# Performance work log

Hardware: AMD Instinct MI355X
Metric: run time of the kernel (lower is better)

Reference implementation:

```python
import jax, jax.numpy as jnp
import numpy as np
from jax import lax

C = 192; H = W = T = 32; WS = 4; SS = 2; NH = 6; HD = C // NH
N = WS ** 3; NB = 4; HIDDEN = 4 * C; OUT = 192


def _rel_index():
    c = np.stack(np.meshgrid(np.arange(WS), np.arange(WS), np.arange(WS), indexing='ij')).reshape(3, -1)
    r = (c[:, :, None] - c[:, None, :]).transpose(1, 2, 0) + (WS - 1)
    return (r[..., 0] * (2 * WS - 1) ** 2 + r[..., 1] * (2 * WS - 1) + r[..., 2]).astype(np.int32)  # (N,N)


def _attn_mask():
    m = np.zeros((H, W, T), np.float32)
    sl = [slice(0, -WS), slice(-WS, -SS), slice(-SS, None)]
    cnt = 0
    for hs in sl:
        for ws_ in sl:
            for ts in sl:
                m[hs, ws_, ts] = cnt
                cnt += 1
    mw = m.reshape(H // WS, WS, W // WS, WS, T // WS, WS).transpose(0, 2, 4, 1, 3, 5).reshape(-1, N)
    am = mw[:, None, :] - mw[:, :, None]  # (nW,N,N)
    return np.where(am != 0, -100.0, 0.0).astype(np.float32)

_RPI = _rel_index()
_MASK = _attn_mask()


def _ln(x, g, b):
    mu = x.mean(-1, keepdims=True)
    v = ((x - mu) ** 2).mean(-1, keepdims=True)
    return (x - mu) / jnp.sqrt(v + 1e-5) * g + b


def _partition(x):  # (B,H,W,T,C) -> (B*nW,N,C)
    b = x.shape[0]
    x = x.reshape(b, H // WS, WS, W // WS, WS, T // WS, WS, C)
    return x.transpose(0, 1, 3, 5, 2, 4, 6, 7).reshape(-1, N, C)


def _reverse(w, b):  # (B*nW,N,C) -> (B,H,W,T,C)
    x = w.reshape(b, H // WS, W // WS, T // WS, WS, WS, WS, C)
    return x.transpose(0, 1, 4, 2, 5, 3, 6, 7).reshape(b, H, W, T, C)


def _swin_block(xf, shifted, p, mask):
    (n1g, n1b, qw, qb, rp, pw, pb, n2g, n2b, f1w, f1b, f2w, f2b) = p
    b = xf.shape[0]
    shortcut = xf
    h = _ln(xf, n1g, n1b).reshape(b, H, W, T, C)
    if shifted:
        h = jnp.roll(h, (-SS, -SS, -SS), (1, 2, 3))
    wins = _partition(h)  # (b*nW,N,C)
    qkv = (wins @ qw + qb).reshape(-1, N, 3, NH, HD).transpose(2, 0, 3, 1, 4)
    q, k, v = qkv[0], qkv[1], qkv[2]  # (b*nW,NH,N,HD)
    attn = jnp.einsum('bhnd,bhmd->bhnm', q * (HD ** -0.5), k)
    attn = attn + rp[_RPI].transpose(2, 0, 1)[None]  # + rel-pos bias (NH,N,N)
    if shifted:
        nW = mask.shape[0]
        attn = (attn.reshape(b, nW, NH, N, N) + mask[None, :, None]).reshape(-1, NH, N, N)
    attn = jax.nn.softmax(attn, -1)
    o = jnp.einsum('bhnm,bhmd->bhnd', attn, v).transpose(0, 2, 1, 3).reshape(-1, N, C)
    o = o @ pw + pb
    h = _reverse(o, b)
    if shifted:
        h = jnp.roll(h, (SS, SS, SS), (1, 2, 3))
    xf = shortcut + h.reshape(b, -1, C)
    z = _ln(xf, n2g, n2b)
    z = jax.nn.gelu(z @ f1w + f1b, approximate=False) @ f2w + f2b
    return xf + z


def _forward(x, norm1_g, norm1_b, qkv_w, qkv_b, rpb, proj_w, proj_b,
             norm2_g, norm2_b, fc1_w, fc1_b, fc2_w, fc2_b,
             dw_w, dw_b, pw_w, pw_b, bn_g, bn_b):
    b = x.shape[0]
    xf = x.reshape(b, C, -1).transpose(0, 2, 1)  # b (h w t) c
    mask = jnp.asarray(_MASK)
    for i in range(NB):
        p = (norm1_g[i], norm1_b[i], qkv_w[i], qkv_b[i], rpb[i], proj_w[i], proj_b[i],
             norm2_g[i], norm2_b[i], fc1_w[i], fc1_b[i], fc2_w[i], fc2_b[i])
        xf = _swin_block(xf, i % 2 == 1, p, mask)
    y = xf.transpose(0, 2, 1).reshape(b, C, H, W, T)
    # refine: depthwise 3x3x3 + pointwise 1x1x1 conv, eval-mode BN (mean 0, var 1), ReLU
    dn = ('NCDHW', 'OIDHW', 'NCDHW')
    y = lax.conv_general_dilated(y, dw_w, (1, 1, 1), [(1, 1)] * 3,
                                 dimension_numbers=dn, feature_group_count=C) + dw_b.reshape(1, -1, 1, 1, 1)
    y = lax.conv_general_dilated(y, pw_w, (1, 1, 1), [(0, 0)] * 3,
                                 dimension_numbers=dn) + pw_b.reshape(1, -1, 1, 1, 1)
    y = y / jnp.sqrt(1.0 + 1e-5) * bn_g.reshape(1, -1, 1, 1, 1) + bn_b.reshape(1, -1, 1, 1, 1)
    return jax.nn.relu(y)


def setup_inputs() -> dict:
    ks = jax.random.split(jax.random.key(0), 12)
    s = 0.02
    return {
        'x': jax.random.normal(ks[0], (2, C, H, W, T), jnp.float32),
        'norm1_g': jnp.ones((NB, C)), 'norm1_b': jnp.zeros((NB, C)),
        'qkv_w': jax.random.normal(ks[1], (NB, C, 3 * C)) * s, 'qkv_b': jnp.zeros((NB, 3 * C)),
        'rpb': jax.random.normal(ks[2], (NB, (2 * WS - 1) ** 3, NH)) * s,
        'proj_w': jax.random.normal(ks[3], (NB, C, C)) * s, 'proj_b': jnp.zeros((NB, C)),
        'norm2_g': jnp.ones((NB, C)), 'norm2_b': jnp.zeros((NB, C)),
        'fc1_w': jax.random.normal(ks[4], (NB, C, HIDDEN)) * s, 'fc1_b': jnp.zeros((NB, HIDDEN)),
        'fc2_w': jax.random.normal(ks[5], (NB, HIDDEN, C)) * s, 'fc2_b': jnp.zeros((NB, C)),
        'dw_w': jax.random.normal(ks[6], (C, 1, 3, 3, 3)) * 0.1, 'dw_b': jnp.zeros((C,)),
        'pw_w': jax.random.normal(ks[7], (OUT, C, 1, 1, 1)) * 0.05, 'pw_b': jnp.zeros((OUT,)),
        'bn_g': jnp.ones((OUT,)), 'bn_b': jnp.zeros((OUT,)),
    }


def reference(x, norm1_g, norm1_b, qkv_w, qkv_b, rpb, proj_w, proj_b,
              norm2_g, norm2_b, fc1_w, fc1_b, fc2_w, fc2_b,
              dw_w, dw_b, pw_w, pw_b, bn_g, bn_b):
    return _forward(x, norm1_g, norm1_b, qkv_w, qkv_b, rpb, proj_w, proj_b,
                    norm2_g, norm2_b, fc1_w, fc1_b, fc2_w, fc2_b,
                    dw_w, dw_b, pw_w, pw_b, bn_g, bn_b)
```

## Files before the change

kernel.cpp:

```cpp
#include <hip/hip_runtime.h>
#include <hip/hip_bf16.h>

#define DI __device__ __forceinline__

typedef short bf16x8 __attribute__((ext_vector_type(8)));
typedef float f32x4 __attribute__((ext_vector_type(4)));
typedef short s16x4 __attribute__((ext_vector_type(4)));

DI short f2bf(float f) {
    __hip_bfloat16 h = __float2bfloat16(f);
    return *reinterpret_cast<short*>(&h);
}

DI void gload_lds16(const short* gsrc, short* ldst) {
    __builtin_amdgcn_global_load_lds(
        (const __attribute__((address_space(1))) void*)gsrc,
        (__attribute__((address_space(3))) void*)ldst, 16, 0, 0);
}

DI int reg3(int p) { return p < 28 ? 0 : (p < 30 ? 1 : 2); }

__global__ __launch_bounds__(256) void transpose_in(const float* __restrict__ x,
                                                    float* __restrict__ xf) {
    __shared__ float tile[32][33];
    int b = blockIdx.z;
    int c0 = blockIdx.y * 32;
    int l0 = blockIdx.x * 32;
    int tx = threadIdx.x, ty = threadIdx.y;
#pragma unroll
    for (int i = 0; i < 32; i += 8)
        tile[ty + i][tx] = x[(long)(b * 192 + c0 + ty + i) * 32768 + l0 + tx];
    __syncthreads();
#pragma unroll
    for (int i = 0; i < 32; i += 8)
        xf[(long)(b * 32768 + l0 + ty + i) * 192 + c0 + tx] = tile[tx][ty + i];
}

__global__ __launch_bounds__(256) void prep_w(const float* __restrict__ qkv_w,
                                              const float* __restrict__ proj_w,
                                              const float* __restrict__ fc1_w,
                                              const float* __restrict__ fc2_w,
                                              const float* __restrict__ pw_w,
                                              short* __restrict__ wt) {
    int i = blockIdx.x * 256 + threadIdx.x;
    float v;
    if (i < 1769472) {
        int b4 = i / 442368, r = i - b4 * 442368;
        if (r < 110592) { int n = r / 192, k = r - n * 192; v = qkv_w[b4 * 110592 + k * 576 + n]; }
        else if (r < 147456) { int r2 = r - 110592; int n = r2 / 192, k = r2 - n * 192; v = proj_w[b4 * 36864 + k * 192 + n]; }
        else if (r < 294912) { int r2 = r - 147456; int n = r2 / 192, k = r2 - n * 192; v = fc1_w[b4 * 147456 + k * 768 + n]; }
        else { int r2 = r - 294912; int n = r2 / 768, k = r2 - n * 768; v = fc2_w[b4 * 147456 + k * 192 + n]; }
        wt[i] = f2bf(v);
    } else {
        int r = i - 1769472;
        wt[i] = f2bf(pw_w[r]);
    }
}

template <bool PART>
__global__ __launch_bounds__(256) void ln_k(const float* __restrict__ xf,
                                            const float* __restrict__ g,
                                            const float* __restrict__ bta,
                                            short* __restrict__ out, int shift) {
    int wv = threadIdx.x >> 6, lane = threadIdx.x & 63;
    int row = blockIdx.x * 4 + wv;
    long src;
    if (PART) {
        int b = row >> 15, r = row & 32767, widx = r >> 6, n = r & 63;
        int wh = widx >> 6, ww = (widx >> 3) & 7, wt = widx & 7;
        int ih = n >> 4, iw = (n >> 2) & 3, it = n & 3;
        int h = ((wh << 2) + ih + shift) & 31;
        int w = ((ww << 2) + iw + shift) & 31;
        int t = ((wt << 2) + it + shift) & 31;
        src = ((long)(b << 15) + (h << 10) + (w << 5) + t) * 192;
    } else {
        src = (long)row * 192;
    }
    float v[3], s = 0.f, sq = 0.f;
#pragma unroll
    for (int j = 0; j < 3; j++) {
        v[j] = xf[src + lane + 64 * j];
        s += v[j];
        sq += v[j] * v[j];
    }
#pragma unroll
    for (int o = 1; o < 64; o <<= 1) {
        s += __shfl_xor(s, o, 64);
        sq += __shfl_xor(sq, o, 64);
    }
    float mu = s * (1.f / 192.f);
    float var = sq * (1.f / 192.f) - mu * mu;
    float rstd = rsqrtf(var + 1e-5f);
    long dst = (long)row * 192;
#pragma unroll
    for (int j = 0; j < 3; j++) {
        int c = lane + 64 * j;
        out[dst + c] = f2bf((v[j] - mu) * rstd * g[c] + bta[c]);
    }
}

template <int MODE>
__global__ __launch_bounds__(256) void gemm_k(
    const short* __restrict__ A, const short* __restrict__ Bt,
    const float* __restrict__ bias,
    short* __restrict__ outB, float* __restrict__ resid, float* __restrict__ outF,
    const float* __restrict__ bng, const float* __restrict__ bnb,
    int M, int N, int K, int shift) {
    __shared__ short As[128 * 64];
    __shared__ short Bs[64 * 64];
    const int tid = threadIdx.x;
    const int nwg = gridDim.x;
    const int wg = ((blockIdx.x & 7) * (nwg >> 3)) + (blockIdx.x >> 3);
    const int tiles_n = N >> 6;
    const int m0 = (wg / tiles_n) << 7;
    const int n0 = (wg % tiles_n) << 6;
    const int wv = tid >> 6, lane = tid & 63;
    const int lr = lane & 15, lg = lane >> 4;
    const int srow = lane >> 3;
    const int scb = ((lane & 7) ^ (lane >> 3)) << 3;

    f32x4 acc[2][4] = {};
    for (int kt = 0; kt < K; kt += 64) {
        __syncthreads();
#pragma unroll
        for (int i = 0; i < 4; i++) {
            int rbase = i * 32 + wv * 8;
            gload_lds16(A + (long)(m0 + rbase + srow) * K + kt + scb, As + rbase * 64);
        }
#pragma unroll
        for (int i = 0; i < 2; i++) {
            int rbase = i * 32 + wv * 8;
            gload_lds16(Bt + (long)(n0 + rbase + srow) * K + kt + scb, Bs + rbase * 64);
        }
        __syncthreads();
#pragma unroll
        for (int ks = 0; ks < 2; ks++) {
            bf16x8 af[2], bfv[4];
            int kb = (ks << 2) + lg;
#pragma unroll
            for (int mi = 0; mi < 2; mi++) {
                int r = (wv << 5) + (mi << 4) + lr;
                af[mi] = *(const bf16x8*)(As + r * 64 + ((kb ^ (r & 7)) << 3));
            }
#pragma unroll
            for (int ni = 0; ni < 4; ni++) {
                int r = (ni << 4) + lr;
                bfv[ni] = *(const bf16x8*)(Bs + r * 64 + ((kb ^ (r & 7)) << 3));
            }
#pragma unroll
            for (int mi = 0; mi < 2; mi++)
#pragma unroll
                for (int ni = 0; ni < 4; ni++)
                    acc[mi][ni] = __builtin_amdgcn_mfma_f32_16x16x32_bf16(
                        af[mi], bfv[ni], acc[mi][ni], 0, 0, 0);
        }
    }

#pragma unroll
    for (int mi = 0; mi < 2; mi++) {
        int rbase = m0 + (wv << 5) + (mi << 4) + (lg << 2);
#pragma unroll
        for (int ni = 0; ni < 4; ni++) {
            int col = n0 + (ni << 4) + lr;
            float bv = bias[col];
            if (MODE == 4) {
                float sc = 0.9999950000374997f * bng[col];
                float bb = bnb[col];
                f32x4 o;
#pragma unroll
                for (int e = 0; e < 4; e++) {
                    float v = (acc[mi][ni][e] + bv) * sc + bb;
                    o[e] = v > 0.f ? v : 0.f;
                }
                int b = rbase >> 15, l = rbase & 32767;
                *(f32x4*)(outF + ((long)(b * 192 + col) << 15) + l) = o;
            } else {
#pragma unroll
                for (int e = 0; e < 4; e++) {
                    int r = rbase + e;
                    float v = acc[mi][ni][e] + bv;
                    if (MODE == 0) {
                        outB[(long)r * N + col] = f2bf(v);
                    } else {
                        int b = r >> 15, rr = r & 32767, widx = rr >> 6, n = rr & 63;
                        int wh = widx >> 6, ww = (widx >> 3) & 7, wt = widx & 7;
                        int ih = n >> 4, iw = (n >> 2) & 3, it = n & 3;
                        int h = ((wh << 2) + ih + shift) & 31;
                        int w = ((ww << 2) + iw + shift) & 31;
                        int t = ((wt << 2) + it + shift) & 31;
                        long tok = (long)(b << 15) + (h << 10) + (w << 5) + t;
                        resid[tok * 192 + col] += v;
                    }
                }
            }
        }
    }
}

__global__ __launch_bounds__(512, 2) void mlp_k(const float* __restrict__ XF,
                                                const short* __restrict__ W1g,
                                                const short* __restrict__ W2g,
                                                const float* __restrict__ b1,
                                                const float* __restrict__ b2,
                                                const float* __restrict__ n2g,
                                                const float* __restrict__ n2b,
                                                float* __restrict__ resid) {
    __shared__ short Wbuf[2][24576];
    __shared__ short Hs[16384];
    const int tid = threadIdx.x;
    const int wv = tid >> 6, lane = tid & 63;
    const int lr = lane & 15, lg = lane >> 4;
    const int mt = ((blockIdx.x & 7) << 5) + (blockIdx.x >> 3);
    const int m0 = mt << 8;
    short* hw = Hs + (wv << 11);

    bf16x8 areg[2][6];
#pragma unroll
    for (int mf = 0; mf < 2; mf++) {
        const float* rp = XF + (long)(m0 + (wv << 5) + (mf << 4) + lr) * 192;
        f32x4 xv[6][2];
        float s = 0.f, sq = 0.f;
#pragma unroll
        for (int kk = 0; kk < 6; kk++)
#pragma unroll
            for (int q = 0; q < 2; q++) {
                xv[kk][q] = *(const f32x4*)(rp + kk * 32 + (lg << 3) + q * 4);
#pragma unroll
                for (int e = 0; e < 4; e++) {
                    s += xv[kk][q][e];
                    sq += xv[kk][q][e] * xv[kk][q][e];
                }
            }
        s += __shfl_xor(s, 16, 64); s += __shfl_xor(s, 32, 64);
        sq += __shfl_xor(sq, 16, 64); sq += __shfl_xor(sq, 32, 64);
        float mu = s * (1.f / 192.f);
        float var = sq * (1.f / 192.f) - mu * mu;
        float rstd = rsqrtf(var + 1e-5f);
#pragma unroll
        for (int kk = 0; kk < 6; kk++) {
            int cb = kk * 32 + (lg << 3);
            f32x4 g0 = *(const f32x4*)(n2g + cb), g1 = *(const f32x4*)(n2g + cb + 4);
            f32x4 b0 = *(const f32x4*)(n2b + cb), b1v = *(const f32x4*)(n2b + cb + 4);
            bf16x8 t;
#pragma unroll
            for (int e = 0; e < 4; e++) {
                t[e] = f2bf((xv[kk][0][e] - mu) * rstd * g0[e] + b0[e]);
                t[e + 4] = f2bf((xv[kk][1][e] - mu) * rstd * g1[e] + b1v[e]);
            }
            areg[mf][kk] = t;
        }
    }

    auto stage = [&](int jc, int buf) {
#pragma unroll
        for (int q = 0; q < 3; q++) {
            int base = (wv * 3 + q) * 512;
            int E = base + lane * 8;
            int row = E / 192;
            int cb = (E - row * 192) >> 3;
            gload_lds16(W1g + (long)(jc * 64 + row) * 192 + ((cb ^ (row & 7)) << 3),
                        &Wbuf[buf][base]);
        }
#pragma unroll
        for (int q = 0; q < 3; q++) {
            int base = (wv * 3 + q) * 512;
            int E = base + lane * 8;
            int row = E >> 6;
            int cb = (E & 63) >> 3;
            gload_lds16(W2g + (long)row * 768 + jc * 64 + ((cb ^ (row & 7)) << 3),
                        &Wbuf[buf][12288 + base]);
        }
    };

    stage(0, 0);
    __syncthreads();

    f32x4 acc[2][12] = {};

    for (int j = 0; j < 12; j++) {
        if (j < 11) stage(j + 1, (j + 1) & 1);
        const short* W1s = Wbuf[j & 1];
        const short* W2s = Wbuf[j & 1] + 12288;

        f32x4 hacc[4][2] = {};
#pragma unroll
        for (int kk = 0; kk < 6; kk++) {
            int cb = (kk << 2) + lg;
            bf16x8 wf[4];
#pragma unroll
            for (int hf = 0; hf < 4; hf++) {
                int r = (hf << 4) + lr;
                wf[hf] = *(const bf16x8*)(W1s + r * 192 + ((cb ^ (r & 7)) << 3));
            }
#pragma unroll
            for (int hf = 0; hf < 4; hf++)
#pragma unroll
                for (int mf = 0; mf < 2; mf++)
                    hacc[hf][mf] = __builtin_amdgcn_mfma_f32_16x16x32_bf16(
                        wf[hf], areg[mf][kk], hacc[hf][mf], 0, 0, 0);
        }

#pragma unroll
        for (int hf = 0; hf < 4; hf++) {
            f32x4 bv = *(const f32x4*)(b1 + j * 64 + (hf << 4) + (lg << 2));
#pragma unroll
            for (int mf = 0; mf < 2; mf++) {
                s16x4 hv;
#pragma unroll
                for (int e = 0; e < 4; e++) {
                    float v = hacc[hf][mf][e] + bv[e];
                    float inner = fmaf(-0.07135481627f, v * v, -1.595769122f);
                    float eterm = __expf(v * inner);
                    float gl = v * __builtin_amdgcn_rcpf(1.f + eterm);
                    hv[e] = f2bf(gl);
                }
                int Mrow = (mf << 4) + lr;
                int blk = (hf << 1) | (lg >> 1);
                *(s16x4*)(hw + Mrow * 64 + ((blk ^ (Mrow & 7)) << 3) + ((lg & 1) << 2)) = hv;
            }
        }
        asm volatile("s_waitcnt lgkmcnt(0)" ::: "memory");

#pragma unroll
        for (int kk = 0; kk < 2; kk++) {
            int cb = (kk << 2) + lg;
            bf16x8 ah[2], bw[12];
#pragma unroll
            for (int mf = 0; mf < 2; mf++) {
                int r = (mf << 4) + lr;
                ah[mf] = *(const bf16x8*)(hw + r * 64 + ((cb ^ (r & 7)) << 3));
            }
#pragma unroll
            for (int nj = 0; nj < 12; nj++) {
                int r = (nj << 4) + lr;
                bw[nj] = *(const bf16x8*)(W2s + r * 64 + ((cb ^ (r & 7)) << 3));
            }
#pragma unroll
            for (int mf = 0; mf < 2; mf++)
#pragma unroll
                for (int nj = 0; nj < 12; nj++)
                    acc[mf][nj] = __builtin_amdgcn_mfma_f32_16x16x32_bf16(
                        ah[mf], bw[nj], acc[mf][nj], 0, 0, 0);
        }
        __syncthreads();
    }

#pragma unroll
    for (int mf = 0; mf < 2; mf++) {
        int rbase = m0 + (wv << 5) + (mf << 4) + (lg << 2);
#pragma unroll
        for (int nj = 0; nj < 12; nj++) {
            int col = (nj << 4) + lr;
            float bv = b2[col];
#pragma unroll
            for (int e = 0; e < 4; e++) {
                long r = rbase + e;
                resid[r * 192 + col] += acc[mf][nj][e] + bv;
            }
        }
    }
}

__global__ __launch_bounds__(256) void attn_k(const short* __restrict__ qkv,
                                              const float* __restrict__ rpb,
                                              short* __restrict__ o, int shifted) {
    __shared__ short lds[4 * 6144];
    const int wv = threadIdx.x >> 6, lane = threadIdx.x & 63;
    short* vT = lds + wv * 6144;
    short* P = lds + wv * 6144 + 2048;
    const int task = blockIdx.x * 4 + wv;
    const int win = task / 6, head = task - win * 6;
    const int lr = lane & 15, lg = lane >> 4;
    const long qbase = (long)win * 64 * 576 + head * 32;

    bf16x8 aq[4], bk[4];
#pragma unroll
    for (int bi = 0; bi < 4; bi++)
        aq[bi] = *(const bf16x8*)(qkv + qbase + (long)((bi << 4) + lr) * 576 + (lg << 3));
#pragma unroll
    for (int bj = 0; bj < 4; bj++)
        bk[bj] = *(const bf16x8*)(qkv + qbase + 192 + (long)((bj << 4) + lr) * 576 + (lg << 3));
    f32x4 s[4][4] = {};
#pragma unroll
    for (int bi = 0; bi < 4; bi++)
#pragma unroll
        for (int bj = 0; bj < 4; bj++)
            s[bi][bj] = __builtin_amdgcn_mfma_f32_16x16x32_bf16(aq[bi], bk[bj], s[bi][bj], 0, 0, 0);

#pragma unroll
    for (int j = 0; j < 4; j++) {
        bf16x8 vv = *(const bf16x8*)(qkv + qbase + 384 + (long)lane * 576 + (j << 3));
#pragma unroll
        for (int e = 0; e < 8; e++) {
            int d = (j << 3) + e;
            vT[d * 64 + (((lane >> 3) ^ (d & 7)) << 3) + (lane & 7)] = vv[e];
        }
    }

    const float SCALE = 0.17677669529663687f;
    int widx = win & 511;
    int wh = widx >> 6, ww = (widx >> 3) & 7, wt = widx & 7;
    int ihm[4], iwm[4], itm[4], lblm[4];
#pragma unroll
    for (int bj = 0; bj < 4; bj++) {
        int m = (bj << 4) + lr;
        ihm[bj] = m >> 4; iwm[bj] = (m >> 2) & 3; itm[bj] = m & 3;
        lblm[bj] = reg3((wh << 2) + ihm[bj]) * 9 + reg3((ww << 2) + iwm[bj]) * 3 + reg3((wt << 2) + itm[bj]);
    }
#pragma unroll
    for (int bi = 0; bi < 4; bi++) {
#pragma unroll
        for (int e = 0; e < 4; e++) {
            int n = (bi << 4) + (lg << 2) + e;
            int ihn = n >> 4, iwn = (n >> 2) & 3, itn = n & 3;
            int lbln = reg3((wh << 2) + ihn) * 9 + reg3((ww << 2) + iwn) * 3 + reg3((wt << 2) + itn);
#pragma unroll
            for (int bj = 0; bj < 4; bj++) {
                int idx = (ihn - ihm[bj] + 3) * 49 + (iwn - iwm[bj] + 3) * 7 + (itn - itm[bj] + 3);
                float bias = rpb[idx * 6 + head];
                float val = s[bi][bj][e] * SCALE + bias;
                if (shifted && lbln != lblm[bj]) val -= 100.f;
                s[bi][bj][e] = val;
            }
        }
    }

#pragma unroll
    for (int bi = 0; bi < 4; bi++) {
#pragma unroll
        for (int e = 0; e < 4; e++) {
            float mx = s[bi][0][e];
#pragma unroll
            for (int bj = 1; bj < 4; bj++) mx = fmaxf(mx, s[bi][bj][e]);
#pragma unroll
            for (int off = 1; off < 16; off <<= 1) mx = fmaxf(mx, __shfl_xor(mx, off, 64));
            float sm = 0.f;
#pragma unroll
            for (int bj = 0; bj < 4; bj++) {
                float p = __expf(s[bi][bj][e] - mx);
                s[bi][bj][e] = p;
                sm += p;
            }
#pragma unroll
            for (int off = 1; off < 16; off <<= 1) sm += __shfl_xor(sm, off, 64);
            float rinv = 1.f / sm;
            int n = (bi << 4) + (lg << 2) + e;
#pragma unroll
            for (int bj = 0; bj < 4; bj++) {
                int m = (bj << 4) + lr;
                P[n * 64 + (((m >> 3) ^ (n & 7)) << 3) + (m & 7)] = f2bf(s[bi][bj][e] * rinv);
            }
        }
    }

    f32x4 oacc[4][2] = {};
#pragma unroll
    for (int ks = 0; ks < 2; ks++) {
        bf16x8 ap[4], bv2[2];
        int kb = (ks << 2) + lg;
#pragma unroll
        for (int bi = 0; bi < 4; bi++) {
            int r = (bi << 4) + lr;
            ap[bi] = *(const bf16x8*)(P + r * 64 + ((kb ^ (r & 7)) << 3));
        }
#pragma unroll
        for (int nf = 0; nf < 2; nf++) {
            int d = (nf << 4) + lr;
            bv2[nf] = *(const bf16x8*)(vT + d * 64 + ((kb ^ (d & 7)) << 3));
        }
#pragma unroll
        for (int bi = 0; bi < 4; bi++)
#pragma unroll
            for (int nf = 0; nf < 2; nf++)
                oacc[bi][nf] = __builtin_amdgcn_mfma_f32_16x16x32_bf16(ap[bi], bv2[nf], oacc[bi][nf], 0, 0, 0);
    }
#pragma unroll
    for (int bi = 0; bi < 4; bi++)
#pragma unroll
        for (int nf = 0; nf < 2; nf++)
#pragma unroll
            for (int e = 0; e < 4; e++) {
                int n = (bi << 4) + (lg << 2) + e;
                int d = (nf << 4) + lr;
                o[((long)win * 64 + n) * 192 + head * 32 + d] = f2bf(oacc[bi][nf][e]);
            }
}

__global__ __launch_bounds__(192) void dw_k(const float* __restrict__ xf,
                                            const float* __restrict__ w,
                                            const float* __restrict__ db,
                                            short* __restrict__ out) {
    int c = threadIdx.x;
    int blk = blockIdx.x;
    int t0 = (blk & 3) << 3;
    int bhw = blk >> 2;
    int b = bhw >> 10, h = (bhw >> 5) & 31, wq = bhw & 31;

    float wr[27];
#pragma unroll
    for (int k = 0; k < 27; k++) wr[k] = w[c * 27 + k];
    float bias = db[c];
    float acc[8];
#pragma unroll
    for (int j = 0; j < 8; j++) acc[j] = bias;

#pragma unroll
    for (int a = 0; a < 3; a++) {
        int hh = h + a - 1;
        if (hh < 0 || hh > 31) continue;
#pragma unroll
        for (int bb = 0; bb < 3; bb++) {
            int ww = wq + bb - 1;
            if (ww < 0 || ww > 31) continue;
            const float* base = xf + ((long)(b << 15) + (hh << 10) + (ww << 5)) * 192 + c;
            float val[10];
#pragma unroll
            for (int tt = 0; tt < 10; tt++) {
                int t = t0 + tt - 1;
                val[tt] = (t >= 0 && t < 32) ? base[t * 192] : 0.f;
            }
#pragma unroll
            for (int d = 0; d < 3; d++) {
                float wv = wr[a * 9 + bb * 3 + d];
#pragma unroll
                for (int j = 0; j < 8; j++)
                    acc[j] = fmaf(val[j + d], wv, acc[j]);
            }
        }
    }
    long obase = ((long)(b << 15) + (h << 10) + (wq << 5) + t0) * 192 + c;
#pragma unroll
    for (int j = 0; j < 8; j++) out[obase + j * 192] = f2bf(acc[j]);
}

extern "C" void kernel_launch(void* const* d_in, const int* in_sizes, int n_in,
                              void* d_out, int out_size, void* d_ws, size_t ws_size,
                              hipStream_t stream) {
    const float* x      = (const float*)d_in[0];
    const float* n1g    = (const float*)d_in[1];
    const float* n1b    = (const float*)d_in[2];
    const float* qkv_w  = (const float*)d_in[3];
    const float* qkv_b  = (const float*)d_in[4];
    const float* rpb    = (const float*)d_in[5];
    const float* proj_w = (const float*)d_in[6];
    const float* proj_b = (const float*)d_in[7];
    const float* n2g    = (const float*)d_in[8];
    const float* n2b    = (const float*)d_in[9];
    const float* fc1_w  = (const float*)d_in[10];
    const float* fc1_b  = (const float*)d_in[11];
    const float* fc2_w  = (const float*)d_in[12];
    const float* fc2_b  = (const float*)d_in[13];
    const float* dw_w   = (const float*)d_in[14];
    const float* dw_b   = (const float*)d_in[15];
    const float* pw_w   = (const float*)d_in[16];
    const float* pw_b   = (const float*)d_in[17];
    const float* bn_g   = (const float*)d_in[18];
    const float* bn_b   = (const float*)d_in[19];
    float* outF = (float*)d_out;

    char* ws = (char*)d_ws;
    float* XF = (float*)ws;
    short* Abuf = (short*)(ws + 50331648);
    short* Bbuf = (short*)(ws + 150994944);
    short* WT = (short*)(ws + 226492416);

    transpose_in<<<dim3(1024, 6, 2), dim3(32, 8), 0, stream>>>(x, XF);
    prep_w<<<7056, 256, 0, stream>>>(qkv_w, proj_w, fc1_w, fc2_w, pw_w, WT);

    for (int i = 0; i < 4; i++) {
        int shifted = i & 1;
        int shift = shifted ? 2 : 0;
        ln_k<true><<<16384, 256, 0, stream>>>(XF, n1g + i * 192, n1b + i * 192, Abuf, shift);
        gemm_k<0><<<4608, 256, 0, stream>>>(Abuf, WT + (long)i * 442368, qkv_b + i * 576,
                                            Bbuf, nullptr, nullptr, nullptr, nullptr,
                                            65536, 576, 192, 0);
        attn_k<<<1536, 256, 0, stream>>>(Bbuf, rpb + i * 2058, Abuf, shifted);
        gemm_k<3><<<1536, 256, 0, stream>>>(Abuf, WT + (long)i * 442368 + 110592, proj_b + i * 192,
                                            nullptr, XF, nullptr, nullptr, nullptr,
                                            65536, 192, 192, shift);
        mlp_k<<<256, 512, 0, stream>>>(XF, WT + (long)i * 442368 + 147456,
                                       WT + (long)i * 442368 + 294912,
                                       fc1_b + i * 768, fc2_b + i * 192,
                                       n2g + i * 192, n2b + i * 192, XF);
    }

    dw_k<<<8192, 192, 0, stream>>>(XF, dw_w, dw_b, Abuf);
    gemm_k<4><<<1536, 256, 0, stream>>>(Abuf, WT + 1769472, pw_b,
                                        nullptr, nullptr, outF, bn_g, bn_b,
                                        65536, 192, 192, 0);
}
```

Measured before the change: 766.5 us.

## Fuse LayerNorm into QKV GEMM and use full-weight-resident GEMMs for K=192

Replaces the separate LayerNorm kernel plus generic QKV GEMM with one kernel that loads window-partitioned rows, normalizes them in registers, keeps the A tile in registers and streams 64-column weight chunks through double-buffered LDS. The proj and final pointwise GEMMs become a kernel that holds the entire 192x192 weight in LDS and computes all 192 output columns per 128-row tile, so A is read once. This removes the LN round trip through global memory, one launch per block, and repeated A reloads across N tiles, at the cost of fewer, larger workgroups (512) with more registers and LDS per block.

```diff
diff --git a/kernel.cpp b/kernel.cpp
--- a/kernel.cpp
+++ b/kernel.cpp
@@ -57,111 +57,173 @@
     }
 }
 
-template <bool PART>
-__global__ __launch_bounds__(256) void ln_k(const float* __restrict__ xf,
-                                            const float* __restrict__ g,
-                                            const float* __restrict__ bta,
-                                            short* __restrict__ out, int shift) {
-    int wv = threadIdx.x >> 6, lane = threadIdx.x & 63;
-    int row = blockIdx.x * 4 + wv;
-    long src;
-    if (PART) {
+__global__ __launch_bounds__(256) void qkv_k(const float* __restrict__ XF,
+                                             const short* __restrict__ Wg,
+                                             const float* __restrict__ bias,
+                                             const float* __restrict__ n1g,
+                                             const float* __restrict__ n1b,
+                                             short* __restrict__ out, int shift) {
+    __shared__ short Ws[2][12288];
+    const int tid = threadIdx.x;
+    const int wv = tid >> 6, lane = tid & 63;
+    const int lr = lane & 15, lg = lane >> 4;
+    const int mt = ((blockIdx.x & 7) << 6) + (blockIdx.x >> 3);
+    const int m0 = mt << 7;
+
+    bf16x8 areg[2][6];
+#pragma unroll
+    for (int mf = 0; mf < 2; mf++) {
+        int row = m0 + (wv << 5) + (mf << 4) + lr;
         int b = row >> 15, r = row & 32767, widx = r >> 6, n = r & 63;
         int wh = widx >> 6, ww = (widx >> 3) & 7, wt = widx & 7;
         int ih = n >> 4, iw = (n >> 2) & 3, it = n & 3;
         int h = ((wh << 2) + ih + shift) & 31;
         int w = ((ww << 2) + iw + shift) & 31;
         int t = ((wt << 2) + it + shift) & 31;
-        src = ((long)(b << 15) + (h << 10) + (w << 5) + t) * 192;
-    } else {
-        src = (long)row * 192;
-    }
-    float v[3], s = 0.f, sq = 0.f;
-#pragma unroll
-    for (int j = 0; j < 3; j++) {
-        v[j] = xf[src + lane + 64 * j];
-        s += v[j];
-        sq += v[j] * v[j];
-    }
-#pragma unroll
-    for (int o = 1; o < 64; o <<= 1) {
-        s += __shfl_xor(s, o, 64);
-        sq += __shfl_xor(sq, o, 64);
-    }
-    float mu = s * (1.f / 192.f);
-    float var = sq * (1.f / 192.f) - mu * mu;
-    float rstd = rsqrtf(var + 1e-5f);
-    long dst = (long)row * 192;
-#pragma unroll
-    for (int j = 0; j < 3; j++) {
-        int c = lane + 64 * j;
-        out[dst + c] = f2bf((v[j] - mu) * rstd * g[c] + bta[c]);
+        const float* rp = XF + ((long)(b << 15) + (h << 10) + (w << 5) + t) * 192;
+        f32x4 xv[6][2];
+        float s = 0.f, sq = 0.f;
+#pragma unroll
+        for (int kk = 0; kk < 6; kk++)
+#pragma unroll
+            for (int q = 0; q < 2; q++) {
+                xv[kk][q] = *(const f32x4*)(rp + kk * 32 + (lg << 3) + q * 4);
+#pragma unroll
+                for (int e = 0; e < 4; e++) {
+                    s += xv[kk][q][e];
+                    sq += xv[kk][q][e] * xv[kk][q][e];
+                }
+            }
+        s += __shfl_xor(s, 16, 64); s += __shfl_xor(s, 32, 64);
+        sq += __shfl_xor(sq, 16, 64); sq += __shfl_xor(sq, 32, 64);
+        float mu = s * (1.f / 192.f);
+        float var = sq * (1.f / 192.f) - mu * mu;
+        float rstd = rsqrtf(var + 1e-5f);
+#pragma unroll
+        for (int kk = 0; kk < 6; kk++) {
+            int cb = kk * 32 + (lg << 3);
+            f32x4 g0 = *(const f32x4*)(n1g + cb), g1 = *(const f32x4*)(n1g + cb + 4);
+            f32x4 b0 = *(const f32x4*)(n1b + cb), b1v = *(const f32x4*)(n1b + cb + 4);
+            bf16x8 tt;
+#pragma unroll
+            for (int e = 0; e < 4; e++) {
+                tt[e] = f2bf((xv[kk][0][e] - mu) * rstd * g0[e] + b0[e]);
+                tt[e + 4] = f2bf((xv[kk][1][e] - mu) * rstd * g1[e] + b1v[e]);
+            }
+            areg[mf][kk] = tt;
+        }
+    }
+
+    auto stage = [&](int jc, int buf) {
+#pragma unroll
+        for (int q = 0; q < 6; q++) {
+            int base = (wv * 6 + q) * 512;
+            int E = base + lane * 8;
+            int row = E / 192;
+            int cb = (E - row * 192) >> 3;
+            gload_lds16(Wg + (long)(jc * 64 + row) * 192 + ((cb ^ (row & 7)) << 3),
+                        &Ws[buf][base]);
+        }
+    };
+
+    stage(0, 0);
+    __syncthreads();
+
+    for (int j = 0; j < 9; j++) {
+        if (j < 8) stage(j + 1, (j + 1) & 1);
+        const short* W = Ws[j & 1];
+        f32x4 acc[2][4] = {};
+#pragma unroll
+        for (int kk = 0; kk < 6; kk++) {
+            int cb = (kk << 2) + lg;
+            bf16x8 wf[4];
+#pragma unroll
+            for (int nf = 0; nf < 4; nf++) {
+                int r = (nf << 4) + lr;
+                wf[nf] = *(const bf16x8*)(W + r * 192 + ((cb ^ (r & 7)) << 3));
+            }
+#pragma unroll
+            for (int mf = 0; mf < 2; mf++)
+#pragma unroll
+                for (int nf = 0; nf < 4; nf++)
+                    acc[mf][nf] = __builtin_amdgcn_mfma_f32_16x16x32_bf16(
+                        areg[mf][kk], wf[nf], acc[mf][nf], 0, 0, 0);
+        }
+#pragma unroll
+        for (int mf = 0; mf < 2; mf++) {
+#pragma unroll
+            for (int nf = 0; nf < 4; nf++) {
+                int col = j * 64 + (nf << 4) + lr;
+                float bv = bias[col];
+#pragma unroll
+                for (int e = 0; e < 4; e++) {
+                    int row = m0 + (wv << 5) + (mf << 4) + (lg << 2) + e;
+                    out[(long)row * 576 + col] = f2bf(acc[mf][nf][e] + bv);
+                }
+            }
+        }
+        __syncthreads();
     }
 }
 
 template <int MODE>
-__global__ __launch_bounds__(256) void gemm_k(
-    const short* __restrict__ A, const short* __restrict__ Bt,
-    const float* __restrict__ bias,
-    short* __restrict__ outB, float* __restrict__ resid, float* __restrict__ outF,
-    const float* __restrict__ bng, const float* __restrict__ bnb,
-    int M, int N, int K, int shift) {
-    __shared__ short As[128 * 64];
-    __shared__ short Bs[64 * 64];
+__global__ __launch_bounds__(256) void wk_k(const short* __restrict__ A,
+                                            const short* __restrict__ Wg,
+                                            const float* __restrict__ bias,
+                                            float* __restrict__ resid, float* __restrict__ outF,
+                                            const float* __restrict__ bng,
+                                            const float* __restrict__ bnb, int shift) {
+    __shared__ short Ws[36864];
     const int tid = threadIdx.x;
-    const int nwg = gridDim.x;
-    const int wg = ((blockIdx.x & 7) * (nwg >> 3)) + (blockIdx.x >> 3);
-    const int tiles_n = N >> 6;
-    const int m0 = (wg / tiles_n) << 7;
-    const int n0 = (wg % tiles_n) << 6;
     const int wv = tid >> 6, lane = tid & 63;
     const int lr = lane & 15, lg = lane >> 4;
-    const int srow = lane >> 3;
-    const int scb = ((lane & 7) ^ (lane >> 3)) << 3;
-
-    f32x4 acc[2][4] = {};
-    for (int kt = 0; kt < K; kt += 64) {
-        __syncthreads();
-#pragma unroll
-        for (int i = 0; i < 4; i++) {
-            int rbase = i * 32 + wv * 8;
-            gload_lds16(A + (long)(m0 + rbase + srow) * K + kt + scb, As + rbase * 64);
-        }
-#pragma unroll
-        for (int i = 0; i < 2; i++) {
-            int rbase = i * 32 + wv * 8;
-            gload_lds16(Bt + (long)(n0 + rbase + srow) * K + kt + scb, Bs + rbase * 64);
-        }
-        __syncthreads();
-#pragma unroll
-        for (int ks = 0; ks < 2; ks++) {
-            bf16x8 af[2], bfv[4];
-            int kb = (ks << 2) + lg;
-#pragma unroll
-            for (int mi = 0; mi < 2; mi++) {
-                int r = (wv << 5) + (mi << 4) + lr;
-                af[mi] = *(const bf16x8*)(As + r * 64 + ((kb ^ (r & 7)) << 3));
-            }
-#pragma unroll
-            for (int ni = 0; ni < 4; ni++) {
-                int r = (ni << 4) + lr;
-                bfv[ni] = *(const bf16x8*)(Bs + r * 64 + ((kb ^ (r & 7)) << 3));
-            }
-#pragma unroll
-            for (int mi = 0; mi < 2; mi++)
-#pragma unroll
-                for (int ni = 0; ni < 4; ni++)
-                    acc[mi][ni] = __builtin_amdgcn_mfma_f32_16x16x32_bf16(
-                        af[mi], bfv[ni], acc[mi][ni], 0, 0, 0);
-        }
-    }
-
-#pragma unroll
-    for (int mi = 0; mi < 2; mi++) {
-        int rbase = m0 + (wv << 5) + (mi << 4) + (lg << 2);
-#pragma unroll
-        for (int ni = 0; ni < 4; ni++) {
-            int col = n0 + (ni << 4) + lr;
+    const int mt = ((blockIdx.x & 7) << 6) + (blockIdx.x >> 3);
+    const int m0 = mt << 7;
+
+    bf16x8 areg[2][6];
+#pragma unroll
+    for (int mf = 0; mf < 2; mf++)
+#pragma unroll
+        for (int kk = 0; kk < 6; kk++)
+            areg[mf][kk] = *(const bf16x8*)(A + (long)(m0 + (wv << 5) + (mf << 4) + lr) * 192 + kk * 32 + (lg << 3));
+
+#pragma unroll
+    for (int q = 0; q < 18; q++) {
+        int base = (wv * 18 + q) * 512;
+        int E = base + lane * 8;
+        int row = E / 192;
+        int cb = (E - row * 192) >> 3;
+        gload_lds16(Wg + (long)row * 192 + ((cb ^ (row & 7)) << 3), Ws + base);
+    }
+    __syncthreads();
+
+    f32x4 acc[2][12] = {};
+#pragma unroll
+    for (int kk = 0; kk < 6; kk++) {
+        int cb = (kk << 2) + lg;
+#pragma unroll
+        for (int njb = 0; njb < 3; njb++) {
+            bf16x8 wf[4];
+#pragma unroll
+            for (int q = 0; q < 4; q++) {
+                int r = ((njb * 4 + q) << 4) + lr;
+                wf[q] = *(const bf16x8*)(Ws + r * 192 + ((cb ^ (r & 7)) << 3));
+            }
+#pragma unroll
+            for (int mf = 0; mf < 2; mf++)
+#pragma unroll
+                for (int q = 0; q < 4; q++)
+                    acc[mf][njb * 4 + q] = __builtin_amdgcn_mfma_f32_16x16x32_bf16(
+                        areg[mf][kk], wf[q], acc[mf][njb * 4 + q], 0, 0, 0);
+        }
+    }
+
+#pragma unroll
+    for (int mf = 0; mf < 2; mf++) {
+        int rbase = m0 + (wv << 5) + (mf << 4) + (lg << 2);
+#pragma unroll
+        for (int nj = 0; nj < 12; nj++) {
+            int col = (nj << 4) + lr;
             float bv = bias[col];
             if (MODE == 4) {
                 float sc = 0.9999950000374997f * bng[col];
@@ -169,7 +231,7 @@
                 f32x4 o;
 #pragma unroll
                 for (int e = 0; e < 4; e++) {
-                    float v = (acc[mi][ni][e] + bv) * sc + bb;
+                    float v = (acc[mf][nj][e] + bv) * sc + bb;
                     o[e] = v > 0.f ? v : 0.f;
                 }
                 int b = rbase >> 15, l = rbase & 32767;
@@ -178,19 +240,14 @@
 #pragma unroll
                 for (int e = 0; e < 4; e++) {
                     int r = rbase + e;
-                    float v = acc[mi][ni][e] + bv;
-                    if (MODE == 0) {
-                        outB[(long)r * N + col] = f2bf(v);
-                    } else {
-                        int b = r >> 15, rr = r & 32767, widx = rr >> 6, n = rr & 63;
-                        int wh = widx >> 6, ww = (widx >> 3) & 7, wt = widx & 7;
-                        int ih = n >> 4, iw = (n >> 2) & 3, it = n & 3;
-                        int h = ((wh << 2) + ih + shift) & 31;
-                        int w = ((ww << 2) + iw + shift) & 31;
-                        int t = ((wt << 2) + it + shift) & 31;
-                        long tok = (long)(b << 15) + (h << 10) + (w << 5) + t;
-                        resid[tok * 192 + col] += v;
-                    }
+                    int b = r >> 15, rr = r & 32767, widx = rr >> 6, n = rr & 63;
+                    int wh = widx >> 6, ww = (widx >> 3) & 7, wt = widx & 7;
+                    int ih = n >> 4, iw = (n >> 2) & 3, it = n & 3;
+                    int h = ((wh << 2) + ih + shift) & 31;
+                    int w = ((ww << 2) + iw + shift) & 31;
+                    int t = ((wt << 2) + it + shift) & 31;
+                    long tok = (long)(b << 15) + (h << 10) + (w << 5) + t;
+                    resid[tok * 192 + col] += acc[mf][nj][e] + bv;
                 }
             }
         }
@@ -570,14 +627,11 @@
     for (int i = 0; i < 4; i++) {
         int shifted = i & 1;
         int shift = shifted ? 2 : 0;
-        ln_k<true><<<16384, 256, 0, stream>>>(XF, n1g + i * 192, n1b + i * 192, Abuf, shift);
-        gemm_k<0><<<4608, 256, 0, stream>>>(Abuf, WT + (long)i * 442368, qkv_b + i * 576,
-                                            Bbuf, nullptr, nullptr, nullptr, nullptr,
-                                            65536, 576, 192, 0);
+        qkv_k<<<512, 256, 0, stream>>>(XF, WT + (long)i * 442368, qkv_b + i * 576,
+                                       n1g + i * 192, n1b + i * 192, Bbuf, shift);
         attn_k<<<1536, 256, 0, stream>>>(Bbuf, rpb + i * 2058, Abuf, shifted);
-        gemm_k<3><<<1536, 256, 0, stream>>>(Abuf, WT + (long)i * 442368 + 110592, proj_b + i * 192,
-                                            nullptr, XF, nullptr, nullptr, nullptr,
-                                            65536, 192, 192, shift);
+        wk_k<3><<<512, 256, 0, stream>>>(Abuf, WT + (long)i * 442368 + 110592, proj_b + i * 192,
+                                         XF, nullptr, nullptr, nullptr, shift);
         mlp_k<<<256, 512, 0, stream>>>(XF, WT + (long)i * 442368 + 147456,
                                        WT + (long)i * 442368 + 294912,
                                        fc1_b + i * 768, fc2_b + i * 192,
@@ -585,7 +639,6 @@
     }
 
     dw_k<<<8192, 192, 0, stream>>>(XF, dw_w, dw_b, Abuf);
-    gemm_k<4><<<1536, 256, 0, stream>>>(Abuf, WT + 1769472, pw_b,
-                                        nullptr, nullptr, outF, bn_g, bn_b,
-                                        65536, 192, 192, 0);
-}
+    wk_k<4><<<512, 256, 0, stream>>>(Abuf, WT + 1769472, pw_b,
+                                     nullptr, outF, bn_g, bn_b, 0);
+}
```

Result: faster. 709.4 us, median of 2 (-7.5%).
